# Kernel tuning notes

Measured on AMD Instinct MI355X. Metric: run time of the kernel, lower is better.

The kernel has to match this reference:

```python
import jax, jax.numpy as jnp
import numpy as np

B, T, I, H = 64, 2048, 64, 256


def setup_inputs() -> dict:
    key = jax.random.key(0)
    ks = jax.random.split(key, 7)
    s_ih = 1.0 / np.sqrt(H)
    return {
        "x": jax.random.normal(ks[0], (B, T, I), dtype=jnp.float32),
        "W_ih": jax.random.normal(ks[1], (H, I), dtype=jnp.float32) * s_ih,
        "W_hh": jax.random.normal(ks[2], (H, H), dtype=jnp.float32) * s_ih,
        "b_ih": jax.random.normal(ks[3], (H,), dtype=jnp.float32) * s_ih,
        "b_hh": jax.random.normal(ks[4], (H,), dtype=jnp.float32) * s_ih,
        "W_fc": jax.random.normal(ks[5], (1, H), dtype=jnp.float32) * s_ih,
        "b_fc": jax.random.normal(ks[6], (1,), dtype=jnp.float32) * s_ih,
    }


def reference(x, W_ih, W_hh, b_ih, b_hh, W_fc, b_fc):
    # Precompute input projection for all timesteps: [B,T,H]
    pre = jnp.einsum('bti,hi->bth', x, W_ih) + b_ih + b_hh
    pre_t = jnp.swapaxes(pre, 0, 1)  # [T,B,H]

    def step(h, p_t):
        h_new = jnp.tanh(p_t + h @ W_hh.T)
        return h_new, h_new

    h0 = jnp.zeros((x.shape[0], W_hh.shape[0]), dtype=x.dtype)
    _, hs = jax.lax.scan(step, h0, pre_t)  # hs: [T,B,H]
    out = jnp.swapaxes(hs, 0, 1)  # [B,T,H]
    return out @ W_fc.T + b_fc  # [B,T,1]
```

## Files before the change

kernel.cpp:

```cpp
#include <hip/hip_runtime.h>

#define BB 64
#define TT 2048
#define II 64
#define HH 256
#define NTHR 256

typedef __fp16 h2_t __attribute__((ext_vector_type(2)));
typedef __fp16 h8_t __attribute__((ext_vector_type(8)));

#define H2(i) __builtin_bit_cast(h2_t, (i))
#define I32(h) __builtin_bit_cast(int, (h))

#if __has_builtin(__builtin_amdgcn_fdot2)
#define FDOT2(a, b, c) __builtin_amdgcn_fdot2((a), (b), (c), false)
#else
__device__ __forceinline__ float FDOT2(h2_t a, h2_t b, float c) {
    return fmaf((float)a[0], (float)b[0], fmaf((float)a[1], (float)b[1], c));
}
#endif

__device__ __forceinline__ float ftanh(float x) {
    float e = __expf(2.0f * x);
    return 1.0f - 2.0f * __builtin_amdgcn_rcpf(e + 1.0f);
}

template <int CTRL>
__device__ __forceinline__ float dpp_add(float v) {
    int s = __builtin_amdgcn_update_dpp(0, __float_as_int(v), CTRL, 0xF, 0xF, true);
    return v + __int_as_float(s);
}
template <int CTRL>
__device__ __forceinline__ float dpp_get(float v) {
    int s = __builtin_amdgcn_update_dpp(0, __float_as_int(v), CTRL, 0xF, 0xF, true);
    return __int_as_float(s);
}

__device__ __forceinline__ float mrg4(float a, float b, int lane) {
    float t = (lane & 4) ? b : a;
    float u = (lane & 4) ? a : b;
    float r4  = dpp_get<0x124>(u);
    float r12 = dpp_get<0x12C>(u);
    return t + ((lane & 4) ? r4 : r12);
}
__device__ __forceinline__ float mrg2(float a, float b, int lane) {
    float t = (lane & 2) ? b : a;
    float u = (lane & 2) ? a : b;
    return t + dpp_get<0x4E>(u);
}
__device__ __forceinline__ float mrg1(float a, float b, int lane) {
    float t = (lane & 1) ? b : a;
    float u = (lane & 1) ? a : b;
    return t + dpp_get<0xB1>(u);
}

__launch_bounds__(NTHR, 1)
__global__ void rnn_fused(const float* __restrict__ x,
                          const float* __restrict__ W_ih,
                          const float* __restrict__ W_hh,
                          const float* __restrict__ b_ih,
                          const float* __restrict__ b_hh,
                          const float* __restrict__ W_fc,
                          const float* __restrict__ b_fc,
                          float* __restrict__ out) {
    __shared__ __align__(16) __fp16 hbuf[2][4][64];
    __shared__ float part[TT + 1][8];

    const int tid  = threadIdx.x;
    const int b    = blockIdx.x;
    const int lane = tid & 63;
    const int w    = tid >> 6;
    const int o    = lane >> 3;
    const int q    = lane & 7;

    int whh_i[8][16];
    int wih_i[8][4];
#pragma unroll
    for (int r = 0; r < 8; ++r) {
        const int t_r = w * 64 + o * 8 + r;
#pragma unroll
        for (int c = 0; c < 4; ++c) {
            const float4* wr = (const float4*)(W_hh + t_r * HH + c * 64 + q * 8);
            const float4 wa = wr[0], wb = wr[1];
            whh_i[r][c * 4 + 0] = I32(__builtin_amdgcn_cvt_pkrtz(wa.x, wa.y));
            whh_i[r][c * 4 + 1] = I32(__builtin_amdgcn_cvt_pkrtz(wa.z, wa.w));
            whh_i[r][c * 4 + 2] = I32(__builtin_amdgcn_cvt_pkrtz(wb.x, wb.y));
            whh_i[r][c * 4 + 3] = I32(__builtin_amdgcn_cvt_pkrtz(wb.z, wb.w));
        }
        const float4* wi = (const float4*)(W_ih + t_r * II + q * 8);
        const float4 wa = wi[0], wb = wi[1];
        wih_i[r][0] = I32(__builtin_amdgcn_cvt_pkrtz(wa.x, wa.y));
        wih_i[r][1] = I32(__builtin_amdgcn_cvt_pkrtz(wa.z, wa.w));
        wih_i[r][2] = I32(__builtin_amdgcn_cvt_pkrtz(wb.x, wb.y));
        wih_i[r][3] = I32(__builtin_amdgcn_cvt_pkrtz(wb.z, wb.w));
    }
#pragma unroll
    for (int j = 0; j < 128; ++j) asm volatile("" : "+v"(((int*)whh_i)[j]));
#pragma unroll
    for (int j = 0; j < 32; ++j) asm volatile("" : "+v"(((int*)wih_i)[j]));

    const int myrow = w * 64 + lane;
    const float bias = b_ih[myrow] + b_hh[myrow];
    const float wfc  = W_fc[myrow];
    const float bfc  = b_fc[0];

    for (int idx = tid; idx < 2 * 256; idx += NTHR) ((__fp16*)hbuf)[idx] = (__fp16)0.0f;
    __syncthreads();

    const float* xbase = x + (size_t)b * TT * II + q * 8;
    float* outb = out + (size_t)b * TT;

    char* hb0 = (char*)&hbuf[0][0][0];
    char* hb1 = (char*)&hbuf[1][0][0];
    __fp16* hw0 = (__fp16*)(hb0 + w * 128 + lane * 2);
    __fp16* hw1 = (__fp16*)(hb1 + w * 128 + lane * 2);
    const char* hq0 = hb0 + q * 16;
    const char* hq1 = hb1 + q * 16;

    h2_t xc[4];
    float4 sAa, sAc, sBa, sBc;
    {
        const float4* xp = (const float4*)(xbase);
        const float4 a = xp[0], c = xp[1];
        xc[0] = __builtin_amdgcn_cvt_pkrtz(a.x, a.y);
        xc[1] = __builtin_amdgcn_cvt_pkrtz(a.z, a.w);
        xc[2] = __builtin_amdgcn_cvt_pkrtz(c.x, c.y);
        xc[3] = __builtin_amdgcn_cvt_pkrtz(c.z, c.w);
        const float4* x1 = (const float4*)(xbase + II);
        sAa = x1[0]; sAc = x1[1];
        const float4* x2 = (const float4*)(xbase + 2 * II);
        sBa = x2[0]; sBc = x2[1];
    }

    float hn_prev = 0.0f;

#define STEP(IDX, HRD, HWOUT, SA, SC)                                          \
    {                                                                          \
           \
        const h8_t hv0 = *(const h8_t*)((HRD) + 0 * 128);                      \
        const h8_t hv1 = *(const h8_t*)((HRD) + 1 * 128);                      \
        const h8_t hv2 = *(const h8_t*)((HRD) + 2 * 128);                      \
        const h8_t hv3 = *(const h8_t*)((HRD) + 3 * 128);                      \
           \
        {                                                                      \
            float hc = hn_prev * wfc;                                          \
            hc = dpp_add<0xB1>(hc);                                    \
            hc = dpp_add<0x4E>(hc);                                    \
            hc = dpp_add<0x141>(hc);                  \
            hc = dpp_add<0x140>(hc);                   \
            hc = dpp_add<0x142>(hc);       \
            if ((lane & 31) == 16) part[IDX][w * 2 + (lane >> 5)] = hc;        \
        }                                                                      \
              \
        float a0, a1, a2, a3, a4, a5, a6, a7;                                  \
        a0 = FDOT2(H2(wih_i[0][0]), xc[0], 0.0f);                              \
        a1 = FDOT2(H2(wih_i[1][0]), xc[0], 0.0f);                              \
        a2 = FDOT2(H2(wih_i[2][0]), xc[0], 0.0f);                              \
        a3 = FDOT2(H2(wih_i[3][0]), xc[0], 0.0f);                              \
        a4 = FDOT2(H2(wih_i[4][0]), xc[0], 0.0f);                              \
        a5 = FDOT2(H2(wih_i[5][0]), xc[0], 0.0f);                              \
        a6 = FDOT2(H2(wih_i[6][0]), xc[0], 0.0f);                              \
        a7 = FDOT2(H2(wih_i[7][0]), xc[0], 0.0f);                              \
        _Pragma("unroll")                                                      \
        for (int e = 1; e < 4; ++e) {                                          \
            a0 = FDOT2(H2(wih_i[0][e]), xc[e], a0);                            \
            a1 = FDOT2(H2(wih_i[1][e]), xc[e], a1);                            \
            a2 = FDOT2(H2(wih_i[2][e]), xc[e], a2);                            \
            a3 = FDOT2(H2(wih_i[3][e]), xc[e], a3);                            \
            a4 = FDOT2(H2(wih_i[4][e]), xc[e], a4);                            \
            a5 = FDOT2(H2(wih_i[5][e]), xc[e], a5);                            \
            a6 = FDOT2(H2(wih_i[6][e]), xc[e], a6);                            \
            a7 = FDOT2(H2(wih_i[7][e]), xc[e], a7);                            \
        }                                                                      \
                        \
        xc[0] = __builtin_amdgcn_cvt_pkrtz((SA).x, (SA).y);                    \
        xc[1] = __builtin_amdgcn_cvt_pkrtz((SA).z, (SA).w);                    \
        xc[2] = __builtin_amdgcn_cvt_pkrtz((SC).x, (SC).y);                    \
        xc[3] = __builtin_amdgcn_cvt_pkrtz((SC).z, (SC).w);                    \
        {                                                                      \
            const int rn = ((IDX) + 3 < TT) ? ((IDX) + 3) : (TT - 1);          \
            const float4* xp = (const float4*)(xbase + rn * II);               \
            (SA) = xp[0]; (SC) = xp[1];                                        \
        }                                                                      \
             \
        _Pragma("unroll")                                                      \
        for (int c = 0; c < 4; ++c) {                                          \
            const h8_t hv = (c == 0) ? hv0 : (c == 1) ? hv1                    \
                          : (c == 2) ? hv2 : hv3;                              \
            _Pragma("unroll")                                                  \
            for (int e = 0; e < 4; ++e) {                                      \
                const h2_t he = (e == 0) ? __builtin_shufflevector(hv, hv, 0, 1) \
                              : (e == 1) ? __builtin_shufflevector(hv, hv, 2, 3) \
                              : (e == 2) ? __builtin_shufflevector(hv, hv, 4, 5) \
                                         : __builtin_shufflevector(hv, hv, 6, 7); \
                const int j = c * 4 + e;                                       \
                a0 = FDOT2(H2(whh_i[0][j]), he, a0);                           \
                a1 = FDOT2(H2(whh_i[1][j]), he, a1);                           \
                a2 = FDOT2(H2(whh_i[2][j]), he, a2);                           \
                a3 = FDOT2(H2(whh_i[3][j]), he, a3);                           \
                a4 = FDOT2(H2(whh_i[4][j]), he, a4);                           \
                a5 = FDOT2(H2(whh_i[5][j]), he, a5);                           \
                a6 = FDOT2(H2(whh_i[6][j]), he, a6);                           \
                a7 = FDOT2(H2(whh_i[7][j]), he, a7);                           \
            }                                                                  \
        }                                                                      \
                            \
        const float A0 = mrg4(a0, a4, lane);                                   \
        const float A1 = mrg4(a1, a5, lane);                                   \
        const float A2 = mrg4(a2, a6, lane);                                   \
        const float A3 = mrg4(a3, a7, lane);                                   \
        const float B0 = mrg2(A0, A2, lane);                                   \
        const float B1 = mrg2(A1, A3, lane);                                   \
        const float C0 = mrg1(B0, B1, lane);                                   \
        const float hn = ftanh(C0 + bias);                                     \
        (HWOUT)[0] = (__fp16)hn;                                               \
        hn_prev = hn;                                                          \
                   \
        asm volatile("s_waitcnt lgkmcnt(0)\n\ts_barrier" ::: "memory");        \
    }

    for (int ib = 0; ib < TT; ib += 2) {
        STEP(ib, hq0, hw1, sAa, sAc)
        STEP(ib + 1, hq1, hw0, sBa, sBc)
    }
#undef STEP

    {
        float hc = hn_prev * wfc;
        hc = dpp_add<0xB1>(hc);
        hc = dpp_add<0x4E>(hc);
        hc = dpp_add<0x141>(hc);
        hc = dpp_add<0x140>(hc);
        hc = dpp_add<0x142>(hc);
        if ((lane & 31) == 16) part[TT][w * 2 + (lane >> 5)] = hc;
    }
    __syncthreads();

    for (int i = tid; i < TT; i += NTHR) {
        const float4* pp = (const float4*)&part[i + 1][0];
        const float4 s0 = pp[0], s1 = pp[1];
        outb[i] = s0.x + s0.y + s0.z + s0.w + s1.x + s1.y + s1.z + s1.w + bfc;
    }
}

extern "C" void kernel_launch(void* const* d_in, const int* in_sizes, int n_in,
                              void* d_out, int out_size, void* d_ws, size_t ws_size,
                              hipStream_t stream) {
    const float* x    = (const float*)d_in[0];
    const float* W_ih = (const float*)d_in[1];
    const float* W_hh = (const float*)d_in[2];
    const float* b_ih = (const float*)d_in[3];
    const float* b_hh = (const float*)d_in[4];
    const float* W_fc = (const float*)d_in[5];
    const float* b_fc = (const float*)d_in[6];
    float* out = (float*)d_out;

    rnn_fused<<<BB, NTHR, 0, stream>>>(x, W_ih, W_hh, b_ih, b_hh, W_fc, b_fc, out);
}
```

Before: 1.137 ms.

## Pack two batch sequences per workgroup sharing one barrier

Each workgroup now runs two independent batch rows with 512 threads: two groups of four waves, each with its own hidden-state double buffer and partial-sum array. The grid shrinks to 32 blocks, which halves the number of CUs in use. Every step's s_barrier now synchronises eight waves instead of four, so the two recurrences are coupled and each step waits for the slower group. The intent is presumably to interleave two sequences on one CU to hide latency, at the cost of a heavier barrier and more register and LDS pressure per CU.

```diff
diff --git a/kernel.cpp b/kernel.cpp
--- a/kernel.cpp
+++ b/kernel.cpp
@@ -1,10 +1,10 @@
 #include <hip/hip_runtime.h>
 
-#define BB 64
+#define BB 32
 #define TT 2048
 #define II 64
 #define HH 256
-#define NTHR 256
+#define NTHR 512
 
 typedef __fp16 h2_t __attribute__((ext_vector_type(2)));
 typedef __fp16 h8_t __attribute__((ext_vector_type(8)));
@@ -54,7 +54,7 @@
     return t + dpp_get<0xB1>(u);
 }
 
-__launch_bounds__(NTHR, 1)
+__launch_bounds__(NTHR, 2)
 __global__ void rnn_fused(const float* __restrict__ x,
                           const float* __restrict__ W_ih,
                           const float* __restrict__ W_hh,
@@ -63,13 +63,15 @@
                           const float* __restrict__ W_fc,
                           const float* __restrict__ b_fc,
                           float* __restrict__ out) {
-    __shared__ __align__(16) __fp16 hbuf[2][4][64];
-    __shared__ float part[TT + 1][8];
+    __shared__ __align__(16) __fp16 hbuf[2][2][4][64];
+    __shared__ float part[2][TT + 1][8];
 
     const int tid  = threadIdx.x;
-    const int b    = blockIdx.x;
     const int lane = tid & 63;
-    const int w    = tid >> 6;
+    const int wv   = tid >> 6;
+    const int g    = wv >> 2;
+    const int wg   = wv & 3;
+    const int b    = blockIdx.x * 2 + g;
     const int o    = lane >> 3;
     const int q    = lane & 7;
 
@@ -77,7 +79,7 @@
     int wih_i[8][4];
 #pragma unroll
     for (int r = 0; r < 8; ++r) {
-        const int t_r = w * 64 + o * 8 + r;
+        const int t_r = wg * 64 + o * 8 + r;
 #pragma unroll
         for (int c = 0; c < 4; ++c) {
             const float4* wr = (const float4*)(W_hh + t_r * HH + c * 64 + q * 8);
@@ -99,23 +101,24 @@
 #pragma unroll
     for (int j = 0; j < 32; ++j) asm volatile("" : "+v"(((int*)wih_i)[j]));
 
-    const int myrow = w * 64 + lane;
+    const int myrow = wg * 64 + lane;
     const float bias = b_ih[myrow] + b_hh[myrow];
     const float wfc  = W_fc[myrow];
     const float bfc  = b_fc[0];
 
-    for (int idx = tid; idx < 2 * 256; idx += NTHR) ((__fp16*)hbuf)[idx] = (__fp16)0.0f;
+    for (int idx = tid; idx < 2 * 2 * 256; idx += NTHR)
+        ((__fp16*)hbuf)[idx] = (__fp16)0.0f;
     __syncthreads();
 
     const float* xbase = x + (size_t)b * TT * II + q * 8;
     float* outb = out + (size_t)b * TT;
-
-    char* hb0 = (char*)&hbuf[0][0][0];
-    char* hb1 = (char*)&hbuf[1][0][0];
-    __fp16* hw0 = (__fp16*)(hb0 + w * 128 + lane * 2);
-    __fp16* hw1 = (__fp16*)(hb1 + w * 128 + lane * 2);
-    const char* hq0 = hb0 + q * 16;
-    const char* hq1 = hb1 + q * 16;
+    float (*partg)[8] = part[g];
+
+    char* hbg = (char*)&hbuf[g][0][0][0];
+    __fp16* hw0 = (__fp16*)(hbg + 0 * 512 + wg * 128 + lane * 2);
+    __fp16* hw1 = (__fp16*)(hbg + 1 * 512 + wg * 128 + lane * 2);
+    const char* hq0 = hbg + 0 * 512 + q * 16;
+    const char* hq1 = hbg + 1 * 512 + q * 16;
 
     h2_t xc[4];
     float4 sAa, sAc, sBa, sBc;
@@ -149,7 +152,7 @@
             hc = dpp_add<0x141>(hc);                  \
             hc = dpp_add<0x140>(hc);                   \
             hc = dpp_add<0x142>(hc);       \
-            if ((lane & 31) == 16) part[IDX][w * 2 + (lane >> 5)] = hc;        \
+            if ((lane & 31) == 16) partg[IDX][wg * 2 + (lane >> 5)] = hc;      \
         }                                                                      \
               \
         float a0, a1, a2, a3, a4, a5, a6, a7;                                  \
@@ -215,7 +218,8 @@
         const float hn = ftanh(C0 + bias);                                     \
         (HWOUT)[0] = (__fp16)hn;                                               \
         hn_prev = hn;                                                          \
-                   \
+           \
+                        \
         asm volatile("s_waitcnt lgkmcnt(0)\n\ts_barrier" ::: "memory");        \
     }
 
@@ -232,12 +236,13 @@
         hc = dpp_add<0x141>(hc);
         hc = dpp_add<0x140>(hc);
         hc = dpp_add<0x142>(hc);
-        if ((lane & 31) == 16) part[TT][w * 2 + (lane >> 5)] = hc;
+        if ((lane & 31) == 16) partg[TT][wg * 2 + (lane >> 5)] = hc;
     }
     __syncthreads();
 
-    for (int i = tid; i < TT; i += NTHR) {
-        const float4* pp = (const float4*)&part[i + 1][0];
+    const int tg = tid & 255;
+    for (int i = tg; i < TT; i += 256) {
+        const float4* pp = (const float4*)&partg[i + 1][0];
         const float4 s0 = pp[0], s1 = pp[1];
         outb[i] = s0.x + s0.y + s0.z + s0.w + s1.x + s1.y + s1.z + s1.w + bfc;
     }
```

Result: slower. 1.929 ms (+69.7%).
